# Kernel optimization log

Hardware: AMD Instinct MI355X
Metric: run time of the kernel (lower is better)

## Reference

```python
import jax, jax.numpy as jnp
import numpy as np

N = 100_000   # nodes
E = 1_000_000 # edges
D_IN = 64
H = 64
G = 64        # graphs in batch
OUT = 2


def gcn_conv(x, edge_index, W, b):
    # PyG GCNConv: add self-loops, symmetric D^-1/2 (A+I) D^-1/2 normalization
    h = x @ W                                   # [N, H]
    src, dst = edge_index[0], edge_index[1]
    n = x.shape[0]
    deg = jax.ops.segment_sum(jnp.ones(E, x.dtype), dst, num_segments=n) + 1.0  # +1 self loop
    dinv = jax.lax.rsqrt(deg)                   # [N]
    norm = dinv[src] * dinv[dst]                # [E]
    msg = h[src] * norm[:, None]                # gather + scale [E, H]
    agg = jax.ops.segment_sum(msg, dst, num_segments=n)
    agg = agg + h * (dinv * dinv)[:, None]      # self-loop term
    return agg + b


def setup_inputs() -> dict:
    key = jax.random.key(0)
    ks = jax.random.split(key, 8)
    x = jax.random.normal(ks[0], (N, D_IN), jnp.float32)
    edge_index = jax.random.randint(ks[1], (2, E), 0, N, dtype=jnp.int64)
    batch = jnp.sort(jax.random.randint(ks[2], (N,), 0, G, dtype=jnp.int64))
    graph_feats = jax.random.normal(ks[3], (G, 1), jnp.float32)
    W1 = jax.random.normal(ks[4], (D_IN, H), jnp.float32) / np.sqrt(D_IN)
    b1 = jnp.zeros((H,), jnp.float32)
    W2 = jax.random.normal(ks[5], (H, H), jnp.float32) / np.sqrt(H)
    b2 = jnp.zeros((H,), jnp.float32)
    Wlin = jax.random.normal(ks[6], (H + 1, OUT), jnp.float32) / np.sqrt(H + 1)
    blin = jnp.zeros((OUT,), jnp.float32)
    return {"x": x, "edge_index": edge_index, "batch": batch,
            "graph_feats": graph_feats, "W1": W1, "b1": b1,
            "W2": W2, "b2": b2, "Wlin": Wlin, "blin": blin}


def reference(x, edge_index, batch, graph_feats, W1, b1, W2, b2, Wlin, blin):
    h = jax.nn.relu(gcn_conv(x, edge_index, W1, b1))
    # dropout is identity in eval mode
    h = jax.nn.relu(gcn_conv(h, edge_index, W2, b2))
    pooled = jax.ops.segment_sum(h, batch, num_segments=G)  # global_add_pool [G, H]
    feats = jnp.concatenate([pooled, graph_feats], axis=1)  # [G, H+1]
    return feats @ Wlin + blin
```

## Files before the change

### kernel.cpp

```cpp
#include <hip/hip_runtime.h>

#define H 64
#define G 64
#define OUT 2
#define MAXBUK 128
#define BSHIFT 10
#define CAP 12288
#define CAPE 1024

typedef unsigned int uint32;
using short8 = __attribute__((ext_vector_type(8))) short;
using f32x4  = __attribute__((ext_vector_type(4))) float;

union ABFrag { uint32 u[4]; uint4 q; short8 v; };

__device__ inline float bf16lo(uint32 u) { return __uint_as_float(u << 16); }
__device__ inline float bf16hi(uint32 u) { return __uint_as_float(u & 0xffff0000u); }
__device__ inline uint32 packbf16(float a, float b) {
    uint32 ua = __float_as_uint(a);
    uint32 ub = __float_as_uint(b);
    ua = (ua + 0x7fffu + ((ua >> 16) & 1u)) >> 16;
    ub = (ub + 0x7fffu + ((ub >> 16) & 1u)) & 0xffff0000u;
    return ua | ub;
}

__global__ __launch_bounds__(256) void k_setup(const float* __restrict__ W1,
                                               const float* __restrict__ W2,
                                               uint32* __restrict__ Wb,
                                               float* __restrict__ pooled,
                                               int* __restrict__ bcnt,
                                               int* __restrict__ done) {
    int blk = blockIdx.x;
    int t = threadIdx.x;
    if (blk < 2) {
        const float* W = blk ? W2 : W1;
        uint32* dw = Wb + blk * 2048;
        for (int i = t; i < 2048; i += 256) {
            int r = i & 3;
            int lane = (i >> 2) & 63;
            int slot = i >> 8;
            int ct = slot >> 1, ks = slot & 1;
            int col = ct * 16 + (lane & 15);
            int k0 = ks * 32 + (lane >> 4) * 8;
            float a = W[(k0 + 2 * r) * 64 + col];
            float b = W[(k0 + 2 * r + 1) * 64 + col];
            dw[i] = packbf16(a, b);
        }
    } else {
        for (int i = t; i < G * H; i += 256) pooled[i] = 0.0f;
        if (t < MAXBUK) bcnt[t] = 0;
        if (t == 0) *done = 0;
    }
}

__global__ __launch_bounds__(256) void k_bhist(const int* __restrict__ dst,
                                               int* __restrict__ bcnt,
                                               int* __restrict__ bbase,
                                               int* __restrict__ bcur,
                                               int* __restrict__ done,
                                               int e, int nbuk) {
    __shared__ int hh[MAXBUK];
    for (int i = threadIdx.x; i < MAXBUK; i += 256) hh[i] = 0;
    __syncthreads();
    int stride = gridDim.x * 256;
    for (int i = blockIdx.x * 256 + threadIdx.x; i < e; i += stride)
        atomicAdd(&hh[__builtin_nontemporal_load(&dst[i]) >> BSHIFT], 1);
    __syncthreads();
    for (int i = threadIdx.x; i < nbuk; i += 256)
        if (hh[i]) atomicAdd(&bcnt[i], hh[i]);
    if (threadIdx.x == 0) {
        __threadfence();
        int ticket = atomicAdd(done, 1);
        if (ticket == (int)gridDim.x - 1) {
            int run = 0;
            for (int i = 0; i < nbuk; ++i) {
                int c = atomicAdd(&bcnt[i], 0);
                bbase[i] = run; bcur[i] = run; run += c;
            }
            bbase[nbuk] = run;
        }
    }
}

__global__ __launch_bounds__(256) void k_bscatter(const int* __restrict__ src,
                                                  const int* __restrict__ dst,
                                                  int* __restrict__ bcur,
                                                  uint32* __restrict__ inter, int e) {
    __shared__ int cnt[MAXBUK];
    __shared__ int run[MAXBUK];
    int per = (e + gridDim.x - 1) / gridDim.x;
    int lo = blockIdx.x * per, hi = min(lo + per, e);
    for (int i = threadIdx.x; i < MAXBUK; i += 256) cnt[i] = 0;
    __syncthreads();
    for (int i = lo + threadIdx.x; i < hi; i += 256)
        atomicAdd(&cnt[dst[i] >> BSHIFT], 1);
    __syncthreads();
    if (threadIdx.x < MAXBUK) {
        int c = cnt[threadIdx.x];
        run[threadIdx.x] = c ? atomicAdd(&bcur[threadIdx.x], c) : 0;
        cnt[threadIdx.x] = 0;
    }
    __syncthreads();
    for (int i = lo + threadIdx.x; i < hi; i += 256) {
        int d = dst[i];
        int s = src[i];
        int b = d >> BSHIFT;
        int ln = d & ((1 << BSHIFT) - 1);
        int pos = run[b] + atomicAdd(&cnt[b], 1);
        inter[pos] = ((uint32)ln << 17) | (uint32)s;
    }
}

__global__ __launch_bounds__(256) void k_build(const uint32* __restrict__ inter,
                                               const int* __restrict__ bbase,
                                               int* __restrict__ rowptr,
                                               float* __restrict__ dinv,
                                               int* __restrict__ csr,
                                               int n, int nbuk) {
    __shared__ int cnt[1024];
    __shared__ int scn[1024];
    __shared__ int part[256];
    __shared__ int stage[CAP];
    int b = blockIdx.x;
    int t = threadIdx.x;
    int nlo = b << BSHIFT;
    int nhi = min(nlo + 1024, n);
    int nn = nhi - nlo;
    int e0 = bbase[b], e1 = bbase[b + 1];
    int ne = e1 - e0;
    for (int i = t; i < nn; i += 256) cnt[i] = 0;
    __syncthreads();
    for (int i = t; i < ne; i += 256)
        atomicAdd(&cnt[inter[e0 + i] >> 17], 1);
    __syncthreads();
    int base4 = 4 * t;
    int sum = 0;
    for (int j = 0; j < 4; ++j) {
        int idx = base4 + j;
        int v = (idx < nn) ? cnt[idx] : 0;
        if (idx < nn) scn[idx] = sum;
        sum += v;
    }
    part[t] = sum;
    __syncthreads();
    for (int off = 1; off < 256; off <<= 1) {
        int v = (t >= off) ? part[t - off] : 0;
        __syncthreads();
        part[t] += v;
        __syncthreads();
    }
    int pbase = (t == 0) ? 0 : part[t - 1];
    for (int j = 0; j < 4; ++j) {
        int idx = base4 + j;
        if (idx < nn) scn[idx] += pbase;
    }
    __syncthreads();
    for (int i = t; i < nn; i += 256) {
        rowptr[nlo + i] = e0 + scn[i];
        dinv[nlo + i] = rsqrtf((float)cnt[i] + 1.0f);
    }
    if (b == 0 && t == 0) rowptr[n] = bbase[nbuk];
    for (int i = t; i < nn; i += 256) cnt[i] = 0;
    __syncthreads();
    for (int i = t; i < ne; i += 256) {
        uint32 p = inter[e0 + i];
        int ln = p >> 17;
        int s = p & 0x1FFFF;
        int pos = scn[ln] + atomicAdd(&cnt[ln], 1);
        if (pos < CAP) stage[pos] = s;
        else csr[e0 + pos] = s;
    }
    __syncthreads();
    int m = min(ne, CAP);
    for (int i = t; i < m; i += 256) csr[e0 + i] = stage[i];
}

template <int BFIN>
__global__ __launch_bounds__(256) void k_gemm_mfma(const void* __restrict__ Xv,
                                                   const uint32* __restrict__ Wb,
                                                   const float* __restrict__ dinv,
                                                   uint32* __restrict__ Y, int n) {
    int lane = threadIdx.x & 63;
    int wave = threadIdx.x >> 6;
    int l15 = lane & 15;
    int grp = lane >> 4;
    ABFrag bf[4][2];
    const uint4* Wb4 = (const uint4*)Wb;
#pragma unroll
    for (int ct = 0; ct < 4; ++ct)
#pragma unroll
        for (int ks = 0; ks < 2; ++ks)
            bf[ct][ks].q = Wb4[(ct * 2 + ks) * 64 + lane];

    int rbase0 = blockIdx.x * 128 + wave * 32;
    f32x4 acc[2][4] = {};
#pragma unroll
    for (int sub = 0; sub < 2; ++sub) {
        int row = min(rbase0 + sub * 16 + l15, n - 1);
        ABFrag a[2];
        if (BFIN) {
            const uint4* X4 = (const uint4*)Xv;
#pragma unroll
            for (int ks = 0; ks < 2; ++ks)
                a[ks].q = X4[(size_t)row * 8 + ks * 4 + grp];
        } else {
            const float4* X4 = (const float4*)Xv;
#pragma unroll
            for (int ks = 0; ks < 2; ++ks) {
                float4 f0 = X4[(size_t)row * 16 + ks * 8 + grp * 2];
                float4 f1 = X4[(size_t)row * 16 + ks * 8 + grp * 2 + 1];
                a[ks].u[0] = packbf16(f0.x, f0.y);
                a[ks].u[1] = packbf16(f0.z, f0.w);
                a[ks].u[2] = packbf16(f1.x, f1.y);
                a[ks].u[3] = packbf16(f1.z, f1.w);
            }
        }
#pragma unroll
        for (int ct = 0; ct < 4; ++ct) {
            acc[sub][ct] = __builtin_amdgcn_mfma_f32_16x16x32_bf16(a[0].v, bf[ct][0].v,
                                                                   acc[sub][ct], 0, 0, 0);
            acc[sub][ct] = __builtin_amdgcn_mfma_f32_16x16x32_bf16(a[1].v, bf[ct][1].v,
                                                                   acc[sub][ct], 0, 0, 0);
        }
    }
#pragma unroll
    for (int sub = 0; sub < 2; ++sub) {
        int rb = rbase0 + sub * 16;
#pragma unroll
        for (int r = 0; r < 4; ++r) {
            int row = rb + grp * 4 + r;
            float dd = dinv[min(row, n - 1)];
#pragma unroll
            for (int ct = 0; ct < 4; ++ct) {
                float v = acc[sub][ct][r] * dd;
                float w = __shfl_xor(v, 1);
                if (!(lane & 1) && row < n)
                    Y[(size_t)row * 32 + ct * 8 + (l15 >> 1)] = packbf16(v, w);
            }
        }
    }
}

template <int DOPOOL>
__global__ __launch_bounds__(256) void k_aggregate(const uint32* __restrict__ h,
                                                   const int* __restrict__ csrs,
                                                   const int* __restrict__ rowptr,
                                                   const float* __restrict__ dinv,
                                                   const float* __restrict__ b,
                                                   const int* __restrict__ batch,
                                                   uint32* __restrict__ hout,
                                                   float* __restrict__ pooled, int n) {
    __shared__ int eidx[CAPE];
    __shared__ int rp[9];
    __shared__ float red[8][64];
    __shared__ int sg[8];
    int tid = threadIdx.x;
    int wave = tid >> 6;
    int lane = tid & 63;
    int half = lane >> 5;
    int hl = lane & 31;
    int grp = hl >> 3;
    int sub = hl & 7;
    int slot = wave * 2 + half;
    int nb = blockIdx.x * 8;
    int node = nb + slot;
    bool active = node < n;
    if (tid < 9) rp[tid] = rowptr[min(nb + tid, n)];
    __syncthreads();
    int e0 = rp[0];
    int ne = rp[8] - e0;
    for (int i = tid; i < ne && i < CAPE; i += 256)
        eidx[i] = csrs[e0 + i];
    __syncthreads();

    const uint4* h4 = (const uint4*)h;
    float acc[8] = {};
    float o[8] = {};
    int r0 = rp[slot], r1 = rp[slot + 1];
    int m = r1 - 1;
    for (int e = r0; e < r1; e += 16) {
        int eA = min(e + grp, m),      eB = min(e + 4 + grp, m);
        int eC = min(e + 8 + grp, m),  eD = min(e + 12 + grp, m);
        int lA = eA - e0, lB = eB - e0, lC = eC - e0, lD = eD - e0;
        int sA = (lA < CAPE) ? eidx[lA] : csrs[eA];
        int sB = (lB < CAPE) ? eidx[lB] : csrs[eB];
        int sC = (lC < CAPE) ? eidx[lC] : csrs[eC];
        int sD = (lD < CAPE) ? eidx[lD] : csrs[eD];
        uint4 gA = h4[(size_t)sA * 8 + sub];
        uint4 gB = h4[(size_t)sB * 8 + sub];
        uint4 gC = h4[(size_t)sC * 8 + sub];
        uint4 gD = h4[(size_t)sD * 8 + sub];
        if (e + grp > m)      { gA.x = gA.y = gA.z = gA.w = 0u; }
        if (e + 4 + grp > m)  { gB.x = gB.y = gB.z = gB.w = 0u; }
        if (e + 8 + grp > m)  { gC.x = gC.y = gC.z = gC.w = 0u; }
        if (e + 12 + grp > m) { gD.x = gD.y = gD.z = gD.w = 0u; }
        acc[0] += bf16lo(gA.x) + bf16lo(gB.x) + bf16lo(gC.x) + bf16lo(gD.x);
        acc[1] += bf16hi(gA.x) + bf16hi(gB.x) + bf16hi(gC.x) + bf16hi(gD.x);
        acc[2] += bf16lo(gA.y) + bf16lo(gB.y) + bf16lo(gC.y) + bf16lo(gD.y);
        acc[3] += bf16hi(gA.y) + bf16hi(gB.y) + bf16hi(gC.y) + bf16hi(gD.y);
        acc[4] += bf16lo(gA.z) + bf16lo(gB.z) + bf16lo(gC.z) + bf16lo(gD.z);
        acc[5] += bf16hi(gA.z) + bf16hi(gB.z) + bf16hi(gC.z) + bf16hi(gD.z);
        acc[6] += bf16lo(gA.w) + bf16lo(gB.w) + bf16lo(gC.w) + bf16lo(gD.w);
        acc[7] += bf16hi(gA.w) + bf16hi(gB.w) + bf16hi(gC.w) + bf16hi(gD.w);
    }
#pragma unroll
    for (int c = 0; c < 8; ++c) {
        acc[c] += __shfl_xor(acc[c], 8);
        acc[c] += __shfl_xor(acc[c], 16);
    }
    if (active && grp == 0) {
        uint4 sv = h4[(size_t)node * 8 + sub];
        float dd = dinv[node];
        o[0] = (acc[0] + bf16lo(sv.x)) * dd + b[hl * 8 + 0];
        o[1] = (acc[1] + bf16hi(sv.x)) * dd + b[hl * 8 + 1];
        o[2] = (acc[2] + bf16lo(sv.y)) * dd + b[hl * 8 + 2];
        o[3] = (acc[3] + bf16hi(sv.y)) * dd + b[hl * 8 + 3];
        o[4] = (acc[4] + bf16lo(sv.z)) * dd + b[hl * 8 + 4];
        o[5] = (acc[5] + bf16hi(sv.z)) * dd + b[hl * 8 + 5];
        o[6] = (acc[6] + bf16lo(sv.w)) * dd + b[hl * 8 + 6];
        o[7] = (acc[7] + bf16hi(sv.w)) * dd + b[hl * 8 + 7];
#pragma unroll
        for (int c = 0; c < 8; ++c) o[c] = o[c] > 0.f ? o[c] : 0.f;
        if (!DOPOOL) {
            uint4 u;
            u.x = packbf16(o[0], o[1]);
            u.y = packbf16(o[2], o[3]);
            u.z = packbf16(o[4], o[5]);
            u.w = packbf16(o[6], o[7]);
            ((uint4*)hout)[(size_t)node * 8 + hl] = u;
        }
    }
    if (DOPOOL) {
        if (grp == 0) {
#pragma unroll
            for (int c = 0; c < 8; ++c)
                red[slot][hl * 8 + c] = active ? o[c] : 0.f;
        }
        if (hl == 0) sg[slot] = active ? batch[node] : -1;
        __syncthreads();
        if (wave == 0) {
            float s = red[0][lane];
            int gcur = sg[0];
            for (int w = 1; w < 8; ++w) {
                int gw = sg[w];
                if (gw < 0) break;
                if (gw == gcur) {
                    s += red[w][lane];
                } else {
                    if (gcur >= 0) atomicAdd(&pooled[gcur * H + lane], s);
                    s = red[w][lane];
                    gcur = gw;
                }
            }
            if (gcur >= 0) atomicAdd(&pooled[gcur * H + lane], s);
        }
    }
}

__global__ void k_final(const float* __restrict__ pooled, const float* __restrict__ gf,
                        const float* __restrict__ Wlin, const float* __restrict__ blin,
                        float* __restrict__ out) {
    int t = threadIdx.x;
    if (t >= G * OUT) return;
    int g = t >> 1, o = t & 1;
    float acc = blin[o];
#pragma unroll
    for (int j = 0; j < 64; ++j) acc += pooled[g * H + j] * Wlin[j * OUT + o];
    acc += gf[g] * Wlin[64 * OUT + o];
    out[g * OUT + o] = acc;
}

extern "C" void kernel_launch(void* const* d_in, const int* in_sizes, int n_in,
                              void* d_out, int out_size, void* d_ws, size_t ws_size,
                              hipStream_t stream) {
    const float* x          = (const float*)d_in[0];
    const int*   edge_index = (const int*)d_in[1];
    const int*   batch      = (const int*)d_in[2];
    const float* gf         = (const float*)d_in[3];
    const float* W1         = (const float*)d_in[4];
    const float* b1         = (const float*)d_in[5];
    const float* W2         = (const float*)d_in[6];
    const float* b2         = (const float*)d_in[7];
    const float* Wlin       = (const float*)d_in[8];
    const float* blin       = (const float*)d_in[9];
    float* out = (float*)d_out;

    const int N = in_sizes[0] / H;
    const int E = in_sizes[1] / 2;
    const int* src = edge_index;
    const int* dst = edge_index + E;
    const int NBUK = (N + (1 << BSHIFT) - 1) >> BSHIFT;

    float* ws = (float*)d_ws;
    float* dinv   = ws;
    uint32* bufA  = (uint32*)(dinv + N);
    uint32* bufB  = bufA + (size_t)N * 32;
    float* pooled = (float*)(bufB + (size_t)N * 32);
    int*   rowptr = (int*)(pooled + G * H);
    int*   bcnt   = rowptr + (N + 1);
    int*   bbase  = bcnt + MAXBUK;
    int*   bcur   = bbase + (MAXBUK + 1);
    int*   done   = bcur + MAXBUK;
    size_t off = (size_t)(done + 1 - (int*)d_ws);
    off = (off + 3) & ~(size_t)3;
    uint32* Wb   = (uint32*)d_ws + off;
    int*   csrs  = (int*)(Wb + 2 * 2048);
    uint32* inter = (uint32*)(csrs + E);

    const int T = 256;

    k_setup<<<3, T, 0, stream>>>(W1, W2, Wb, pooled, bcnt, done);
    k_bhist<<<256, T, 0, stream>>>(dst, bcnt, bbase, bcur, done, E, NBUK);
    k_bscatter<<<128, T, 0, stream>>>(src, dst, bcur, inter, E);
    k_build<<<NBUK, T, 0, stream>>>(inter, bbase, rowptr, dinv, csrs, N, NBUK);

    const int NBG = (N + 127) / 128;

    k_gemm_mfma<0><<<NBG, T, 0, stream>>>(x, Wb, dinv, bufA, N);
    k_aggregate<0><<<(N + 7) / 8, T, 0, stream>>>(bufA, csrs, rowptr, dinv, b1, batch,
                                                  bufB, pooled, N);

    k_gemm_mfma<1><<<NBG, T, 0, stream>>>(bufB, Wb + 2048, dinv, bufA, N);
    k_aggregate<1><<<(N + 7) / 8, T, 0, stream>>>(bufA, csrs, rowptr, dinv, b2, batch,
                                                  nullptr, pooled, N);

    k_final<<<1, 128, 0, stream>>>(pooled, gf, Wlin, blin, out);
}
```

Measured before the change: 171.0 us.

## Fuse layer-1 aggregation with layer-2 GEMM and drop shared edge staging

Layer-1 aggregation now also does the layer-2 dense transform. Each block keeps its 8 aggregated rows in LDS and multiplies them by a 16KB fp32 copy of W2 using scalar FMAs. This removes the separate MFMA GEMM launch and the bf16 round trip of the intermediate features through global memory. The shared-memory staging of edge indices is also dropped in favour of direct csr loads. The trade-off is a W2 reload into LDS for every 8-node block (12.5k blocks) plus extra LDS occupancy and scalar arithmetic, which may cost more than the removed GEMM pass.

```diff
diff --git a/kernel.cpp b/kernel.cpp
--- a/kernel.cpp
+++ b/kernel.cpp
@@ -6,7 +6,6 @@
 #define MAXBUK 128
 #define BSHIFT 10
 #define CAP 12288
-#define CAPE 1024
 
 typedef unsigned int uint32;
 using short8 = __attribute__((ext_vector_type(8))) short;
@@ -25,16 +24,13 @@
 }
 
 __global__ __launch_bounds__(256) void k_setup(const float* __restrict__ W1,
-                                               const float* __restrict__ W2,
                                                uint32* __restrict__ Wb,
                                                float* __restrict__ pooled,
                                                int* __restrict__ bcnt,
                                                int* __restrict__ done) {
     int blk = blockIdx.x;
     int t = threadIdx.x;
-    if (blk < 2) {
-        const float* W = blk ? W2 : W1;
-        uint32* dw = Wb + blk * 2048;
+    if (blk == 0) {
         for (int i = t; i < 2048; i += 256) {
             int r = i & 3;
             int lane = (i >> 2) & 63;
@@ -42,9 +38,9 @@
             int ct = slot >> 1, ks = slot & 1;
             int col = ct * 16 + (lane & 15);
             int k0 = ks * 32 + (lane >> 4) * 8;
-            float a = W[(k0 + 2 * r) * 64 + col];
-            float b = W[(k0 + 2 * r + 1) * 64 + col];
-            dw[i] = packbf16(a, b);
+            float a = W1[(k0 + 2 * r) * 64 + col];
+            float b = W1[(k0 + 2 * r + 1) * 64 + col];
+            Wb[i] = packbf16(a, b);
         }
     } else {
         for (int i = t; i < G * H; i += 256) pooled[i] = 0.0f;
@@ -175,8 +171,7 @@
     for (int i = t; i < m; i += 256) csr[e0 + i] = stage[i];
 }
 
-template <int BFIN>
-__global__ __launch_bounds__(256) void k_gemm_mfma(const void* __restrict__ Xv,
+__global__ __launch_bounds__(256) void k_gemm_mfma(const float* __restrict__ Xv,
                                                    const uint32* __restrict__ Wb,
                                                    const float* __restrict__ dinv,
                                                    uint32* __restrict__ Y, int n) {
@@ -198,22 +193,15 @@
     for (int sub = 0; sub < 2; ++sub) {
         int row = min(rbase0 + sub * 16 + l15, n - 1);
         ABFrag a[2];
-        if (BFIN) {
-            const uint4* X4 = (const uint4*)Xv;
-#pragma unroll
-            for (int ks = 0; ks < 2; ++ks)
-                a[ks].q = X4[(size_t)row * 8 + ks * 4 + grp];
-        } else {
-            const float4* X4 = (const float4*)Xv;
-#pragma unroll
-            for (int ks = 0; ks < 2; ++ks) {
-                float4 f0 = X4[(size_t)row * 16 + ks * 8 + grp * 2];
-                float4 f1 = X4[(size_t)row * 16 + ks * 8 + grp * 2 + 1];
-                a[ks].u[0] = packbf16(f0.x, f0.y);
-                a[ks].u[1] = packbf16(f0.z, f0.w);
-                a[ks].u[2] = packbf16(f1.x, f1.y);
-                a[ks].u[3] = packbf16(f1.z, f1.w);
-            }
+        const float4* X4 = (const float4*)Xv;
+#pragma unroll
+        for (int ks = 0; ks < 2; ++ks) {
+            float4 f0 = X4[(size_t)row * 16 + ks * 8 + grp * 2];
+            float4 f1 = X4[(size_t)row * 16 + ks * 8 + grp * 2 + 1];
+            a[ks].u[0] = packbf16(f0.x, f0.y);
+            a[ks].u[1] = packbf16(f0.z, f0.w);
+            a[ks].u[2] = packbf16(f1.x, f1.y);
+            a[ks].u[3] = packbf16(f1.z, f1.w);
         }
 #pragma unroll
         for (int ct = 0; ct < 4; ++ct) {
@@ -241,19 +229,15 @@
     }
 }
 
-template <int DOPOOL>
-__global__ __launch_bounds__(256) void k_aggregate(const uint32* __restrict__ h,
-                                                   const int* __restrict__ csrs,
-                                                   const int* __restrict__ rowptr,
-                                                   const float* __restrict__ dinv,
-                                                   const float* __restrict__ b,
-                                                   const int* __restrict__ batch,
-                                                   uint32* __restrict__ hout,
-                                                   float* __restrict__ pooled, int n) {
-    __shared__ int eidx[CAPE];
-    __shared__ int rp[9];
-    __shared__ float red[8][64];
-    __shared__ int sg[8];
+__global__ __launch_bounds__(256) void k_agg_gemm(const uint32* __restrict__ h,
+                                                  const int* __restrict__ csrs,
+                                                  const int* __restrict__ rowptr,
+                                                  const float* __restrict__ dinv,
+                                                  const float* __restrict__ b1,
+                                                  const float* __restrict__ W2,
+                                                  uint32* __restrict__ y2, int n) {
+    __shared__ float h1s[8][64];
+    __shared__ float w2s[64][64];
     int tid = threadIdx.x;
     int wave = tid >> 6;
     int lane = tid & 63;
@@ -265,27 +249,25 @@
     int nb = blockIdx.x * 8;
     int node = nb + slot;
     bool active = node < n;
-    if (tid < 9) rp[tid] = rowptr[min(nb + tid, n)];
-    __syncthreads();
-    int e0 = rp[0];
-    int ne = rp[8] - e0;
-    for (int i = tid; i < ne && i < CAPE; i += 256)
-        eidx[i] = csrs[e0 + i];
-    __syncthreads();
+
+    {
+        const float4* W24 = (const float4*)W2;
+        float4* w2s4 = (float4*)&w2s[0][0];
+        for (int i = tid; i < 1024; i += 256) w2s4[i] = W24[i];
+    }
 
     const uint4* h4 = (const uint4*)h;
     float acc[8] = {};
-    float o[8] = {};
-    int r0 = rp[slot], r1 = rp[slot + 1];
+    int r0 = 0, r1 = 0;
+    if (active) { r0 = rowptr[node]; r1 = rowptr[node + 1]; }
     int m = r1 - 1;
     for (int e = r0; e < r1; e += 16) {
         int eA = min(e + grp, m),      eB = min(e + 4 + grp, m);
         int eC = min(e + 8 + grp, m),  eD = min(e + 12 + grp, m);
-        int lA = eA - e0, lB = eB - e0, lC = eC - e0, lD = eD - e0;
-        int sA = (lA < CAPE) ? eidx[lA] : csrs[eA];
-        int sB = (lB < CAPE) ? eidx[lB] : csrs[eB];
-        int sC = (lC < CAPE) ? eidx[lC] : csrs[eC];
-        int sD = (lD < CAPE) ? eidx[lD] : csrs[eD];
+        int sA = csrs[eA];
+        int sB = csrs[eB];
+        int sC = csrs[eC];
+        int sD = csrs[eD];
         uint4 gA = h4[(size_t)sA * 8 + sub];
         uint4 gB = h4[(size_t)sB * 8 + sub];
         uint4 gC = h4[(size_t)sC * 8 + sub];
@@ -311,49 +293,133 @@
     if (active && grp == 0) {
         uint4 sv = h4[(size_t)node * 8 + sub];
         float dd = dinv[node];
-        o[0] = (acc[0] + bf16lo(sv.x)) * dd + b[hl * 8 + 0];
-        o[1] = (acc[1] + bf16hi(sv.x)) * dd + b[hl * 8 + 1];
-        o[2] = (acc[2] + bf16lo(sv.y)) * dd + b[hl * 8 + 2];
-        o[3] = (acc[3] + bf16hi(sv.y)) * dd + b[hl * 8 + 3];
-        o[4] = (acc[4] + bf16lo(sv.z)) * dd + b[hl * 8 + 4];
-        o[5] = (acc[5] + bf16hi(sv.z)) * dd + b[hl * 8 + 5];
-        o[6] = (acc[6] + bf16lo(sv.w)) * dd + b[hl * 8 + 6];
-        o[7] = (acc[7] + bf16hi(sv.w)) * dd + b[hl * 8 + 7];
-#pragma unroll
-        for (int c = 0; c < 8; ++c) o[c] = o[c] > 0.f ? o[c] : 0.f;
-        if (!DOPOOL) {
-            uint4 u;
-            u.x = packbf16(o[0], o[1]);
-            u.y = packbf16(o[2], o[3]);
-            u.z = packbf16(o[4], o[5]);
-            u.w = packbf16(o[6], o[7]);
-            ((uint4*)hout)[(size_t)node * 8 + hl] = u;
-        }
-    }
-    if (DOPOOL) {
-        if (grp == 0) {
-#pragma unroll
-            for (int c = 0; c < 8; ++c)
-                red[slot][hl * 8 + c] = active ? o[c] : 0.f;
-        }
-        if (hl == 0) sg[slot] = active ? batch[node] : -1;
-        __syncthreads();
-        if (wave == 0) {
-            float s = red[0][lane];
-            int gcur = sg[0];
-            for (int w = 1; w < 8; ++w) {
-                int gw = sg[w];
-                if (gw < 0) break;
-                if (gw == gcur) {
-                    s += red[w][lane];
-                } else {
-                    if (gcur >= 0) atomicAdd(&pooled[gcur * H + lane], s);
-                    s = red[w][lane];
-                    gcur = gw;
-                }
+        float o0 = (acc[0] + bf16lo(sv.x)) * dd + b1[hl * 8 + 0];
+        float o1 = (acc[1] + bf16hi(sv.x)) * dd + b1[hl * 8 + 1];
+        float o2 = (acc[2] + bf16lo(sv.y)) * dd + b1[hl * 8 + 2];
+        float o3 = (acc[3] + bf16hi(sv.y)) * dd + b1[hl * 8 + 3];
+        float o4 = (acc[4] + bf16lo(sv.z)) * dd + b1[hl * 8 + 4];
+        float o5 = (acc[5] + bf16hi(sv.z)) * dd + b1[hl * 8 + 5];
+        float o6 = (acc[6] + bf16lo(sv.w)) * dd + b1[hl * 8 + 6];
+        float o7 = (acc[7] + bf16hi(sv.w)) * dd + b1[hl * 8 + 7];
+        h1s[slot][hl * 8 + 0] = o0 > 0.f ? o0 : 0.f;
+        h1s[slot][hl * 8 + 1] = o1 > 0.f ? o1 : 0.f;
+        h1s[slot][hl * 8 + 2] = o2 > 0.f ? o2 : 0.f;
+        h1s[slot][hl * 8 + 3] = o3 > 0.f ? o3 : 0.f;
+        h1s[slot][hl * 8 + 4] = o4 > 0.f ? o4 : 0.f;
+        h1s[slot][hl * 8 + 5] = o5 > 0.f ? o5 : 0.f;
+        h1s[slot][hl * 8 + 6] = o6 > 0.f ? o6 : 0.f;
+        h1s[slot][hl * 8 + 7] = o7 > 0.f ? o7 : 0.f;
+    }
+    __syncthreads();
+    {
+        int r = tid >> 5;
+        int q = tid & 31;
+        int row = nb + r;
+        if (row < n) {
+            float a0 = 0.f, a1 = 0.f;
+#pragma unroll
+            for (int k = 0; k < 64; ++k) {
+                float hv = h1s[r][k];
+                const float2* wrow = (const float2*)w2s[k];
+                float2 wv = wrow[q];
+                a0 += hv * wv.x;
+                a1 += hv * wv.y;
             }
-            if (gcur >= 0) atomicAdd(&pooled[gcur * H + lane], s);
-        }
+            float dd = dinv[row];
+            y2[(size_t)row * 32 + q] = packbf16(a0 * dd, a1 * dd);
+        }
+    }
+}
+
+__global__ __launch_bounds__(256) void k_aggregate2(const uint32* __restrict__ h,
+                                                    const int* __restrict__ csrs,
+                                                    const int* __restrict__ rowptr,
+                                                    const float* __restrict__ dinv,
+                                                    const float* __restrict__ b,
+                                                    const int* __restrict__ batch,
+                                                    float* __restrict__ pooled, int n) {
+    __shared__ float red[8][64];
+    __shared__ int sg[8];
+    int tid = threadIdx.x;
+    int wave = tid >> 6;
+    int lane = tid & 63;
+    int half = lane >> 5;
+    int hl = lane & 31;
+    int grp = hl >> 3;
+    int sub = hl & 7;
+    int slot = wave * 2 + half;
+    int node = blockIdx.x * 8 + slot;
+    bool active = node < n;
+    const uint4* h4 = (const uint4*)h;
+    float acc[8] = {};
+    int r0 = 0, r1 = 0;
+    if (active) { r0 = rowptr[node]; r1 = rowptr[node + 1]; }
+    int m = r1 - 1;
+    for (int e = r0; e < r1; e += 16) {
+        int eA = min(e + grp, m),      eB = min(e + 4 + grp, m);
+        int eC = min(e + 8 + grp, m),  eD = min(e + 12 + grp, m);
+        int sA = csrs[eA];
+        int sB = csrs[eB];
+        int sC = csrs[eC];
+        int sD = csrs[eD];
+        uint4 gA = h4[(size_t)sA * 8 + sub];
+        uint4 gB = h4[(size_t)sB * 8 + sub];
+        uint4 gC = h4[(size_t)sC * 8 + sub];
+        uint4 gD = h4[(size_t)sD * 8 + sub];
+        if (e + grp > m)      { gA.x = gA.y = gA.z = gA.w = 0u; }
+        if (e + 4 + grp > m)  { gB.x = gB.y = gB.z = gB.w = 0u; }
+        if (e + 8 + grp > m)  { gC.x = gC.y = gC.z = gC.w = 0u; }
+        if (e + 12 + grp > m) { gD.x = gD.y = gD.z = gD.w = 0u; }
+        acc[0] += bf16lo(gA.x) + bf16lo(gB.x) + bf16lo(gC.x) + bf16lo(gD.x);
+        acc[1] += bf16hi(gA.x) + bf16hi(gB.x) + bf16hi(gC.x) + bf16hi(gD.x);
+        acc[2] += bf16lo(gA.y) + bf16lo(gB.y) + bf16lo(gC.y) + bf16lo(gD.y);
+        acc[3] += bf16hi(gA.y) + bf16hi(gB.y) + bf16hi(gC.y) + bf16hi(gD.y);
+        acc[4] += bf16lo(gA.z) + bf16lo(gB.z) + bf16lo(gC.z) + bf16lo(gD.z);
+        acc[5] += bf16hi(gA.z) + bf16hi(gB.z) + bf16hi(gC.z) + bf16hi(gD.z);
+        acc[6] += bf16lo(gA.w) + bf16lo(gB.w) + bf16lo(gC.w) + bf16lo(gD.w);
+        acc[7] += bf16hi(gA.w) + bf16hi(gB.w) + bf16hi(gC.w) + bf16hi(gD.w);
+    }
+#pragma unroll
+    for (int c = 0; c < 8; ++c) {
+        acc[c] += __shfl_xor(acc[c], 8);
+        acc[c] += __shfl_xor(acc[c], 16);
+    }
+    if (grp == 0) {
+        float o[8] = {};
+        if (active) {
+            uint4 sv = h4[(size_t)node * 8 + sub];
+            float dd = dinv[node];
+            o[0] = (acc[0] + bf16lo(sv.x)) * dd + b[hl * 8 + 0];
+            o[1] = (acc[1] + bf16hi(sv.x)) * dd + b[hl * 8 + 1];
+            o[2] = (acc[2] + bf16lo(sv.y)) * dd + b[hl * 8 + 2];
+            o[3] = (acc[3] + bf16hi(sv.y)) * dd + b[hl * 8 + 3];
+            o[4] = (acc[4] + bf16lo(sv.z)) * dd + b[hl * 8 + 4];
+            o[5] = (acc[5] + bf16hi(sv.z)) * dd + b[hl * 8 + 5];
+            o[6] = (acc[6] + bf16lo(sv.w)) * dd + b[hl * 8 + 6];
+            o[7] = (acc[7] + bf16hi(sv.w)) * dd + b[hl * 8 + 7];
+#pragma unroll
+            for (int c = 0; c < 8; ++c) o[c] = o[c] > 0.f ? o[c] : 0.f;
+        }
+#pragma unroll
+        for (int c = 0; c < 8; ++c) red[slot][hl * 8 + c] = o[c];
+    }
+    if (hl == 0) sg[slot] = active ? batch[node] : -1;
+    __syncthreads();
+    if (wave == 0) {
+        float s = red[0][lane];
+        int gcur = sg[0];
+        for (int w = 1; w < 8; ++w) {
+            int gw = sg[w];
+            if (gw < 0) break;
+            if (gw == gcur) {
+                s += red[w][lane];
+            } else {
+                if (gcur >= 0) atomicAdd(&pooled[gcur * H + lane], s);
+                s = red[w][lane];
+                gcur = gw;
+            }
+        }
+        if (gcur >= 0) atomicAdd(&pooled[gcur * H + lane], s);
     }
 }
 
@@ -404,25 +470,23 @@
     size_t off = (size_t)(done + 1 - (int*)d_ws);
     off = (off + 3) & ~(size_t)3;
     uint32* Wb   = (uint32*)d_ws + off;
-    int*   csrs  = (int*)(Wb + 2 * 2048);
+    int*   csrs  = (int*)(Wb + 2048);
     uint32* inter = (uint32*)(csrs + E);
 
     const int T = 256;
 
-    k_setup<<<3, T, 0, stream>>>(W1, W2, Wb, pooled, bcnt, done);
+    k_setup<<<2, T, 0, stream>>>(W1, Wb, pooled, bcnt, done);
     k_bhist<<<256, T, 0, stream>>>(dst, bcnt, bbase, bcur, done, E, NBUK);
     k_bscatter<<<128, T, 0, stream>>>(src, dst, bcur, inter, E);
     k_build<<<NBUK, T, 0, stream>>>(inter, bbase, rowptr, dinv, csrs, N, NBUK);
 
-    const int NBG = (N + 127) / 128;
-
-    k_gemm_mfma<0><<<NBG, T, 0, stream>>>(x, Wb, dinv, bufA, N);
-    k_aggregate<0><<<(N + 7) / 8, T, 0, stream>>>(bufA, csrs, rowptr, dinv, b1, batch,
-                                                  bufB, pooled, N);
-
-    k_gemm_mfma<1><<<NBG, T, 0, stream>>>(bufB, Wb + 2048, dinv, bufA, N);
-    k_aggregate<1><<<(N + 7) / 8, T, 0, stream>>>(bufA, csrs, rowptr, dinv, b2, batch,
-                                                  nullptr, pooled, N);
+    k_gemm_mfma<<<(N + 127) / 128, T, 0, stream>>>(x, Wb, dinv, bufA, N);
+
+    k_agg_gemm<<<(N + 7) / 8, T, 0, stream>>>(bufA, csrs, rowptr, dinv, b1, W2,
+                                              bufB, N);
+
+    k_aggregate2<<<(N + 7) / 8, T, 0, stream>>>(bufB, csrs, rowptr, dinv, b2, batch,
+                                                pooled, N);
 
     k_final<<<1, 128, 0, stream>>>(pooled, gf, Wlin, blin, out);
 }
```

Result: slower. 179.2 us (+4.8%).
